# Performance work log

Hardware: AMD Instinct MI355X
Metric: run time of the kernel (lower is better)

Reference implementation:

```python
import jax, jax.numpy as jnp
import numpy as np

N_NODES = 50000
N_EDGES = 800000
N_FEAT = 128
HID = 128
N_LAYER = 3
FC_HID = 256
N_CLASS = 10
N_GRAPHS = 64


def setup_inputs() -> dict:
    key = jax.random.key(0)
    ks = jax.random.split(key, 10)
    x = jax.random.normal(ks[0], (N_NODES, N_FEAT), dtype=jnp.float32)
    edge_index = jax.random.randint(ks[1], (2, N_EDGES), 0, N_NODES, dtype=jnp.int32)
    batch = jnp.sort(jax.random.randint(ks[2], (N_NODES,), 0, N_GRAPHS, dtype=jnp.int32))
    s = 0.05
    # SAGEConv per layer: lin_l acts on mean-aggregated neighbors, lin_r on root.
    Wl = jax.random.normal(ks[3], (N_LAYER, HID, HID), dtype=jnp.float32) * s
    Wr = jax.random.normal(ks[4], (N_LAYER, HID, HID), dtype=jnp.float32) * s
    bl = jnp.zeros((N_LAYER, HID), dtype=jnp.float32)
    fc1_w = jax.random.normal(ks[5], (HID * N_LAYER, FC_HID), dtype=jnp.float32) * s
    fc1_b = jnp.zeros((FC_HID,), dtype=jnp.float32)
    fc2_w = jax.random.normal(ks[6], (FC_HID, N_CLASS), dtype=jnp.float32) * s
    fc2_b = jnp.zeros((N_CLASS,), dtype=jnp.float32)
    return {"x": x, "edge_index": edge_index, "batch": batch,
            "Wl": Wl, "Wr": Wr, "bl": bl,
            "fc1_w": fc1_w, "fc1_b": fc1_b, "fc2_w": fc2_w, "fc2_b": fc2_b}


def reference(x, edge_index, batch, Wl, Wr, bl, fc1_w, fc1_b, fc2_w, fc2_b):
    # normalize edge indices to start at 0 (as in the torch forward)
    ei = edge_index - jnp.min(edge_index)
    src, dst = ei[0], ei[1]
    # in-degree for mean aggregation (clamped to avoid div-by-zero)
    deg = jax.ops.segment_sum(jnp.ones((src.shape[0],), x.dtype), dst,
                              num_segments=N_NODES)
    inv_deg = 1.0 / jnp.maximum(deg, 1.0)[:, None]  # [N,1]
    h = x
    layer_outs = []
    for i in range(N_LAYER):
        # (dropout is identity in eval mode)
        agg = jax.ops.segment_sum(h[src], dst, num_segments=N_NODES) * inv_deg  # [N,H]
        h = jax.nn.relu(agg @ Wl[i] + h @ Wr[i] + bl[i])
        layer_outs.append(h)
    hcat = jnp.concatenate(layer_outs, axis=1)  # [N, H*n_layer]
    # mean pooling per graph
    counts = jax.ops.segment_sum(jnp.ones((N_NODES,), x.dtype), batch,
                                 num_segments=N_GRAPHS)
    pooled = jax.ops.segment_sum(hcat, batch, num_segments=N_GRAPHS)
    pooled = pooled / jnp.maximum(counts, 1.0)[:, None]  # [G, H*n_layer]
    out = jax.nn.relu(pooled @ fc1_w + fc1_b) @ fc2_w + fc2_b  # [G, n_class]
    return out
```

## Files before the change

### kernel.cpp

```cpp
#include <hip/hip_runtime.h>
#include <hip/hip_bf16.h>
#include <limits.h>

#define N_NODES 50000
#define N_EDGES 800000
#define HID 128
#define N_LAYER 3
#define FC_HID 256
#define N_CLASS 10
#define N_GRAPHS 64
#define NBKT 98
#define BIN_NB 256
#define PER_BLK ((N_EDGES + BIN_NB - 1) / BIN_NB)

typedef __attribute__((ext_vector_type(8))) short short8;
typedef __attribute__((ext_vector_type(4))) float f32x4;

__device__ inline unsigned f2bf(float f) {
    unsigned u = __float_as_uint(f);
    return (u + 0x7FFFu + ((u >> 16) & 1u)) >> 16;
}
__device__ inline float bf2f(unsigned b) { return __uint_as_float(b << 16); }

__global__ __launch_bounds__(512) void k_minh(const int* __restrict__ ei,
                                              int* __restrict__ emin,
                                              int* __restrict__ hist) {
    __shared__ int red[512];
    __shared__ int lh[NBKT];
    int t = threadIdx.x;
    if (t < NBKT) lh[t] = 0;
    __syncthreads();
    int e0 = blockIdx.x * PER_BLK, e1 = min(e0 + PER_BLK, N_EDGES);
    int v = INT_MAX;
    for (int j = e0 + t; j < e1; j += 512) {
        int s = ei[j], d = ei[N_EDGES + j];
        v = min(v, min(s, d));
        atomicAdd(&lh[d >> 9], 1);
    }
    red[t] = v;
    __syncthreads();
    for (int off = 256; off > 0; off >>= 1) {
        if (t < off) red[t] = min(red[t], red[t + off]);
        __syncthreads();
    }
    if (t == 0) atomicMin(emin, red[0]);
    if (t < NBKT) hist[blockIdx.x * NBKT + t] = lh[t];
}

__global__ void k_base(const int* __restrict__ hist, int* __restrict__ colex,
                       int* __restrict__ btot) {
    __shared__ int s[BIN_NB];
    int b = blockIdx.x, t = threadIdx.x;
    int v = hist[t * NBKT + b];
    s[t] = v;
    __syncthreads();
    for (int off = 1; off < BIN_NB; off <<= 1) {
        int u = (t >= off) ? s[t - off] : 0;
        __syncthreads();
        s[t] += u;
        __syncthreads();
    }
    colex[t * NBKT + b] = s[t] - v;
    if (t == BIN_NB - 1) btot[b] = s[t];
}

__global__ void k_bscan(const int* __restrict__ btot, int* __restrict__ bboff,
                        int* __restrict__ rp, const int* __restrict__ batch,
                        float* __restrict__ counts) {
    __shared__ int s[128];
    int t = threadIdx.x;
    int v = (t < NBKT) ? btot[t] : 0;
    s[t] = v;
    __syncthreads();
    for (int off = 1; off < 128; off <<= 1) {
        int u = (t >= off) ? s[t - off] : 0;
        __syncthreads();
        s[t] += u;
        __syncthreads();
    }
    if (t < NBKT) bboff[t] = s[t] - v;
    if (t == 127) { bboff[NBKT] = s[127]; rp[N_NODES] = s[127]; }
    if (t < N_GRAPHS) {
        int g = t;
        int lo = 0, hi = N_NODES;
        while (lo < hi) { int mid = (lo + hi) >> 1; if (batch[mid] < g) lo = mid + 1; else hi = mid; }
        int lb = lo;
        lo = lb; hi = N_NODES;
        while (lo < hi) { int mid = (lo + hi) >> 1; if (batch[mid] <= g) lo = mid + 1; else hi = mid; }
        counts[g] = (float)(lo - lb);
    }
}

__global__ __launch_bounds__(512) void k_bin(const int* __restrict__ ei,
                                             const int* __restrict__ emin,
                                             const int* __restrict__ bboff,
                                             const int* __restrict__ colex,
                                             unsigned* __restrict__ ebuf) {
    __shared__ int lcnt[NBKT];
    __shared__ int lbase[NBKT];
    int t = threadIdx.x, blk = blockIdx.x;
    if (t < NBKT) {
        lcnt[t] = 0;
        lbase[t] = bboff[t] + colex[blk * NBKT + t];
    }
    __syncthreads();
    int m = *emin;
    int e0 = blk * PER_BLK, e1 = min(e0 + PER_BLK, N_EDGES);
    for (int j = e0 + t; j < e1; j += 512) {
        int s = ei[j] - m, d = ei[N_EDGES + j];
        int bk = d >> 9;
        int idx = atomicAdd(&lcnt[bk], 1);
        ebuf[lbase[bk] + idx] = ((unsigned)s << 9) | (unsigned)(d & 511);
    }
}

__global__ __launch_bounds__(512) void k_scatter2(const unsigned* __restrict__ ebuf,
                                                  const int* __restrict__ bboff,
                                                  const int* __restrict__ emin,
                                                  int* __restrict__ rp,
                                                  float* __restrict__ invd,
                                                  int* __restrict__ csr) {
    __shared__ int ldeg[512];
    __shared__ int lsc[512];
    __shared__ int lfill[512];
    int b = blockIdx.x, t = threadIdx.x;
    int m = *emin;
    if (b == NBKT) {
        for (int nd = NBKT * 512 - m + t; nd < N_NODES; nd += 512)
            if (nd >= 0) { rp[nd] = N_EDGES; invd[nd] = 1.0f; }
        return;
    }
    ldeg[t] = 0;
    lfill[t] = 0;
    __syncthreads();
    int beg = bboff[b], end = bboff[b + 1];
    for (int e = beg + t; e < end; e += 512)
        atomicAdd(&ldeg[ebuf[e] & 511], 1);
    __syncthreads();
    int v = ldeg[t];
    lsc[t] = v;
    __syncthreads();
    for (int off = 1; off < 512; off <<= 1) {
        int u = (t >= off) ? lsc[t - off] : 0;
        __syncthreads();
        lsc[t] += u;
        __syncthreads();
    }
    int base = beg + lsc[t] - v;
    lsc[t] = base;
    int nd = (b << 9) + t - m;
    if (nd >= 0 && nd < N_NODES) {
        rp[nd] = base;
        invd[nd] = 1.0f / (float)max(v, 1);
    }
    __syncthreads();
    for (int e = beg + t; e < end; e += 512) {
        unsigned p = ebuf[e];
        int loc = p & 511;
        int pos = lsc[loc] + atomicAdd(&lfill[loc], 1);
        csr[pos] = (int)(p >> 9);
    }
}

__global__ void k_cvt(const float* __restrict__ x, unsigned* __restrict__ xb, int n4) {
    int i = blockIdx.x * blockDim.x + threadIdx.x;
    if (i >= n4) return;
    float4 v = *(const float4*)(x + (size_t)i * 4);
    uint2 o;
    o.x = f2bf(v.x) | (f2bf(v.y) << 16);
    o.y = f2bf(v.z) | (f2bf(v.w) << 16);
    *(uint2*)(xb + (size_t)i * 2) = o;
}

__global__ void k_prep(const float* __restrict__ Wl, const float* __restrict__ Wr,
                       unsigned* __restrict__ wlh, unsigned* __restrict__ wll,
                       unsigned* __restrict__ wrh, unsigned* __restrict__ wrl) {
    int b = blockIdx.x;
    int t = threadIdx.x;
    const float* src = (b < 3) ? (Wl + (size_t)b * HID * HID) : (Wr + (size_t)(b - 3) * HID * HID);
    unsigned* dh = (b < 3) ? (wlh + (size_t)b * HID * 64) : (wrh + (size_t)(b - 3) * HID * 64);
    unsigned* dl = (b < 3) ? (wll + (size_t)b * HID * 64) : (wrl + (size_t)(b - 3) * HID * 64);
    for (int i = 0; i < 32; ++i) {
        int u = t * 32 + i;
        int n = u >> 6, kk = u & 63;
        float v0 = src[(size_t)(2 * kk) * HID + n];
        float v1 = src[(size_t)(2 * kk + 1) * HID + n];
        unsigned h0 = f2bf(v0), h1 = f2bf(v1);
        unsigned l0 = f2bf(v0 - bf2f(h0)), l1 = f2bf(v1 - bf2f(h1));
        dh[u] = h0 | (h1 << 16);
        dl[u] = l0 | (l1 << 16);
    }
}

__global__ void k_agg(const unsigned* __restrict__ hb, const int* __restrict__ rp,
                      const int* __restrict__ csr, const float* __restrict__ invd,
                      unsigned* __restrict__ aggb) {
    const int n = blockIdx.x;
    const int lane = threadIdx.x;
    int beg = rp[n], end = rp[n + 1];
    float p0 = 0, p1 = 0, q0 = 0, q1 = 0, r0 = 0, r1 = 0, t0 = 0, t1 = 0;
    int e = beg;
    for (; e + 8 <= end; e += 8) {
        int s0 = csr[e], s1 = csr[e + 1], s2 = csr[e + 2], s3 = csr[e + 3];
        int s4 = csr[e + 4], s5 = csr[e + 5], s6 = csr[e + 6], s7 = csr[e + 7];
        unsigned u0 = hb[(size_t)s0 * 64 + lane];
        unsigned u1 = hb[(size_t)s1 * 64 + lane];
        unsigned u2 = hb[(size_t)s2 * 64 + lane];
        unsigned u3 = hb[(size_t)s3 * 64 + lane];
        unsigned u4 = hb[(size_t)s4 * 64 + lane];
        unsigned u5 = hb[(size_t)s5 * 64 + lane];
        unsigned u6 = hb[(size_t)s6 * 64 + lane];
        unsigned u7 = hb[(size_t)s7 * 64 + lane];
        p0 += __uint_as_float(u0 << 16); p1 += __uint_as_float(u0 & 0xFFFF0000u);
        q0 += __uint_as_float(u1 << 16); q1 += __uint_as_float(u1 & 0xFFFF0000u);
        r0 += __uint_as_float(u2 << 16); r1 += __uint_as_float(u2 & 0xFFFF0000u);
        t0 += __uint_as_float(u3 << 16); t1 += __uint_as_float(u3 & 0xFFFF0000u);
        p0 += __uint_as_float(u4 << 16); p1 += __uint_as_float(u4 & 0xFFFF0000u);
        q0 += __uint_as_float(u5 << 16); q1 += __uint_as_float(u5 & 0xFFFF0000u);
        r0 += __uint_as_float(u6 << 16); r1 += __uint_as_float(u6 & 0xFFFF0000u);
        t0 += __uint_as_float(u7 << 16); t1 += __uint_as_float(u7 & 0xFFFF0000u);
    }
    for (; e < end; ++e) {
        unsigned u = hb[(size_t)csr[e] * 64 + lane];
        p0 += __uint_as_float(u << 16);
        p1 += __uint_as_float(u & 0xFFFF0000u);
    }
    float iv = invd[n];
    unsigned o = f2bf((p0 + q0 + r0 + t0) * iv) | (f2bf((p1 + q1 + r1 + t1) * iv) << 16);
    aggb[(size_t)n * 64 + lane] = o;
}

__global__ __launch_bounds__(256, 4) void k_gemm(
    const unsigned* __restrict__ aggb, const unsigned* __restrict__ hinb,
    const unsigned* __restrict__ wlh, const unsigned* __restrict__ wll,
    const unsigned* __restrict__ wrh, const unsigned* __restrict__ wrl,
    const float* __restrict__ bias, const int* __restrict__ batch,
    unsigned* __restrict__ houtb, float* __restrict__ pooled, int layer) {
    __shared__ float Ts[64 * 132];
    __shared__ int bs[64];
    const int tx = threadIdx.x;
    const int wave = tx >> 6, lane = tx & 63;
    const int row0 = blockIdx.x * 64;
    const int lrow = lane & 15, kgrp = lane >> 4;

    if (tx < 64) {
        int grow = row0 + tx;
        bs[tx] = (grow < N_NODES) ? batch[grow] : -1;
    }

    f32x4 acc[4][2];
#pragma unroll
    for (int m = 0; m < 4; ++m)
#pragma unroll
        for (int n = 0; n < 2; ++n) acc[m][n] = (f32x4){0.f, 0.f, 0.f, 0.f};
    const short8 zf = {0, 0, 0, 0, 0, 0, 0, 0};

    for (int kc = 0; kc < 4; ++kc) {
        const int koff = kc * 16 + kgrp * 4;
        short8 af[4], hf[4];
#pragma unroll
        for (int m = 0; m < 4; ++m) {
            int r = row0 + m * 16 + lrow;
            if (r < N_NODES) {
                af[m] = *(const short8*)(aggb + (size_t)r * 64 + koff);
                hf[m] = *(const short8*)(hinb + (size_t)r * 64 + koff);
            } else {
                af[m] = zf;
                hf[m] = zf;
            }
        }
#pragma unroll
        for (int n = 0; n < 2; ++n) {
            int wn = wave * 2 + n;
            size_t wbase = (size_t)(wn * 16 + lrow) * 64 + koff;
            short8 fl_h = *(const short8*)(wlh + wbase);
            short8 fl_l = *(const short8*)(wll + wbase);
            short8 fr_h = *(const short8*)(wrh + wbase);
            short8 fr_l = *(const short8*)(wrl + wbase);
#pragma unroll
            for (int m = 0; m < 4; ++m) {
                acc[m][n] = __builtin_amdgcn_mfma_f32_16x16x32_bf16(af[m], fl_h, acc[m][n], 0, 0, 0);
                acc[m][n] = __builtin_amdgcn_mfma_f32_16x16x32_bf16(af[m], fl_l, acc[m][n], 0, 0, 0);
                acc[m][n] = __builtin_amdgcn_mfma_f32_16x16x32_bf16(hf[m], fr_h, acc[m][n], 0, 0, 0);
                acc[m][n] = __builtin_amdgcn_mfma_f32_16x16x32_bf16(hf[m], fr_l, acc[m][n], 0, 0, 0);
            }
        }
    }

#pragma unroll
    for (int n = 0; n < 2; ++n) {
        int c = wave * 32 + n * 16 + lrow;
        float bb = bias[c];
#pragma unroll
        for (int m = 0; m < 4; ++m)
#pragma unroll
            for (int reg = 0; reg < 4; ++reg) {
                int r = m * 16 + kgrp * 4 + reg;
                Ts[r * 132 + c] = fmaxf(acc[m][n][reg] + bb, 0.f);
            }
    }
    __syncthreads();

#pragma unroll
    for (int it = 0; it < 4; ++it) {
        int f = it * 256 + tx;
        int r = f >> 4, slot = f & 15;
        int grow = row0 + r;
        if (grow < N_NODES) {
            const float* ts = &Ts[r * 132 + slot * 8];
            uint4 o;
            o.x = f2bf(ts[0]) | (f2bf(ts[1]) << 16);
            o.y = f2bf(ts[2]) | (f2bf(ts[3]) << 16);
            o.z = f2bf(ts[4]) | (f2bf(ts[5]) << 16);
            o.w = f2bf(ts[6]) | (f2bf(ts[7]) << 16);
            *(uint4*)(houtb + (size_t)grow * 64 + slot * 4) = o;
        }
    }

    if (tx < 128) {
        int j = tx;
        float run = 0.f;
        int curb = bs[0];
        for (int r = 0; r < 64; ++r) {
            int bb = bs[r];
            if (bb != curb) {
                if (curb >= 0)
                    atomicAdd(&pooled[(size_t)curb * (HID * N_LAYER) + layer * HID + j], run);
                run = 0.f;
                curb = bb;
            }
            run += Ts[r * 132 + j];
        }
        if (curb >= 0)
            atomicAdd(&pooled[(size_t)curb * (HID * N_LAYER) + layer * HID + j], run);
    }
}

__global__ void k_fc(const float* __restrict__ pooled, const float* __restrict__ counts,
                     const float* __restrict__ fc1w, const float* __restrict__ fc1b,
                     const float* __restrict__ fc2w, const float* __restrict__ fc2b,
                     float* __restrict__ out) {
    __shared__ float pr[HID * N_LAYER];
    __shared__ float a1[FC_HID];
    const int g = blockIdx.x, t = threadIdx.x;
    float invc = 1.0f / fmaxf(counts[g], 1.0f);
    for (int i = t; i < HID * N_LAYER; i += FC_HID)
        pr[i] = pooled[(size_t)g * (HID * N_LAYER) + i] * invc;
    __syncthreads();
    float acc = fc1b[t];
    for (int k = 0; k < HID * N_LAYER; ++k)
        acc = fmaf(pr[k], fc1w[(size_t)k * FC_HID + t], acc);
    a1[t] = fmaxf(acc, 0.f);
    __syncthreads();
    if (t < N_CLASS) {
        float o = fc2b[t];
        for (int k = 0; k < FC_HID; ++k)
            o = fmaf(a1[k], fc2w[(size_t)k * N_CLASS + t], o);
        out[(size_t)g * N_CLASS + t] = o;
    }
}

extern "C" void kernel_launch(void* const* d_in, const int* in_sizes, int n_in,
                              void* d_out, int out_size, void* d_ws, size_t ws_size,
                              hipStream_t stream) {
    const float* x = (const float*)d_in[0];
    const int* ei = (const int*)d_in[1];
    const int* batch = (const int*)d_in[2];
    const float* Wl = (const float*)d_in[3];
    const float* Wr = (const float*)d_in[4];
    const float* bl = (const float*)d_in[5];
    const float* fc1w = (const float*)d_in[6];
    const float* fc1b = (const float*)d_in[7];
    const float* fc2w = (const float*)d_in[8];
    const float* fc2b = (const float*)d_in[9];
    float* out = (float*)d_out;

    char* ws = (char*)d_ws;
    size_t off = 0;
    auto alloc = [&](size_t bytes) {
        void* p = ws + off;
        off += (bytes + 255) & ~size_t(255);
        return p;
    };
    int* emin = (int*)alloc(4);
    float* pooled = (float*)alloc((size_t)N_GRAPHS * HID * N_LAYER * 4);
    int* hist = (int*)alloc((size_t)BIN_NB * NBKT * 4);
    int* colex = (int*)alloc((size_t)BIN_NB * NBKT * 4);
    int* btot = (int*)alloc(NBKT * 4);
    int* bboff = (int*)alloc((NBKT + 1) * 4);
    int* rp = (int*)alloc((N_NODES + 1) * 4);
    float* invd = (float*)alloc(N_NODES * 4);
    float* counts = (float*)alloc(N_GRAPHS * 4);
    unsigned* ebuf = (unsigned*)alloc((size_t)N_EDGES * 4);
    int* csr = (int*)alloc((size_t)N_EDGES * 4);
    unsigned* wlh = (unsigned*)alloc((size_t)N_LAYER * HID * 64 * 4);
    unsigned* wll = (unsigned*)alloc((size_t)N_LAYER * HID * 64 * 4);
    unsigned* wrh = (unsigned*)alloc((size_t)N_LAYER * HID * 64 * 4);
    unsigned* wrl = (unsigned*)alloc((size_t)N_LAYER * HID * 64 * 4);
    unsigned* aggb = (unsigned*)alloc((size_t)N_NODES * 64 * 4);
    unsigned* xb = (unsigned*)alloc((size_t)N_NODES * 64 * 4);
    unsigned* hb1 = (unsigned*)alloc((size_t)N_NODES * 64 * 4);
    unsigned* hb2 = (unsigned*)alloc((size_t)N_NODES * 64 * 4);

    hipMemsetAsync(emin, 0x7F, 4, stream);
    hipMemsetAsync(pooled, 0, (size_t)N_GRAPHS * HID * N_LAYER * 4, stream);

    k_minh<<<BIN_NB, 512, 0, stream>>>(ei, emin, hist);
    k_base<<<NBKT, BIN_NB, 0, stream>>>(hist, colex, btot);
    k_bscan<<<1, 128, 0, stream>>>(btot, bboff, rp, batch, counts);
    k_bin<<<BIN_NB, 512, 0, stream>>>(ei, emin, bboff, colex, ebuf);
    k_scatter2<<<NBKT + 1, 512, 0, stream>>>(ebuf, bboff, emin, rp, invd, csr);
    k_cvt<<<(N_NODES * HID / 4 + 255) / 256, 256, 0, stream>>>(x, xb, N_NODES * HID / 4);
    k_prep<<<6, 256, 0, stream>>>(Wl, Wr, wlh, wll, wrh, wrl);

    const unsigned* hin = xb;
    unsigned* houts[3] = {hb1, hb2, hb1};
    for (int layer = 0; layer < N_LAYER; ++layer) {
        k_agg<<<N_NODES, 64, 0, stream>>>(hin, rp, csr, invd, aggb);
        k_gemm<<<(N_NODES + 63) / 64, 256, 0, stream>>>(
            aggb, hin,
            wlh + (size_t)layer * HID * 64, wll + (size_t)layer * HID * 64,
            wrh + (size_t)layer * HID * 64, wrl + (size_t)layer * HID * 64,
            bl + (size_t)layer * HID, batch, houts[layer], pooled, layer);
        hin = houts[layer];
    }
    k_fc<<<N_GRAPHS, 256, 0, stream>>>(pooled, counts, fc1w, fc1b, fc2w, fc2b, out);
}
```

Before: 277.2 us.

## Split aggregation by feature quarters with four edge lanes per node

The neighbor-mean aggregation now launches one wave per node per quarter of the feature columns. Each wave's 64 lanes cover 16 columns times 4 interleaved edges, and the partial sums are combined with cross-lane shuffles. This gives each wave more independent edge gathers and finer-grained work to hide gather latency and improve load balance. The cost is 64-byte rather than 256-byte row segments per gather, four times as many reads of the row pointers and CSR indices, and extra shuffle work.

```diff
diff --git a/kernel.cpp b/kernel.cpp
--- a/kernel.cpp
+++ b/kernel.cpp
@@ -12,6 +12,7 @@
 #define NBKT 98
 #define BIN_NB 256
 #define PER_BLK ((N_EDGES + BIN_NB - 1) / BIN_NB)
+#define AGG_NB ((N_NODES + 3) / 4)
 
 typedef __attribute__((ext_vector_type(8))) short short8;
 typedef __attribute__((ext_vector_type(4))) float f32x4;
@@ -192,42 +193,39 @@
     }
 }
 
-__global__ void k_agg(const unsigned* __restrict__ hb, const int* __restrict__ rp,
-                      const int* __restrict__ csr, const float* __restrict__ invd,
-                      unsigned* __restrict__ aggb) {
-    const int n = blockIdx.x;
-    const int lane = threadIdx.x;
+__global__ __launch_bounds__(256) void k_agg(const unsigned* __restrict__ hb,
+                                             const int* __restrict__ rp,
+                                             const int* __restrict__ csr,
+                                             const float* __restrict__ invd,
+                                             unsigned* __restrict__ aggb) {
+    const int tx = threadIdx.x;
+    const int wave = tx >> 6, lane = tx & 63;
+    const int q = blockIdx.x / AGG_NB;
+    const int nb = blockIdx.x % AGG_NB;
+    const int n = nb * 4 + wave;
+    const int sub = lane >> 4, fl = lane & 15;
+    const int col = q * 16 + fl;
     int beg = rp[n], end = rp[n + 1];
-    float p0 = 0, p1 = 0, q0 = 0, q1 = 0, r0 = 0, r1 = 0, t0 = 0, t1 = 0;
-    int e = beg;
-    for (; e + 8 <= end; e += 8) {
-        int s0 = csr[e], s1 = csr[e + 1], s2 = csr[e + 2], s3 = csr[e + 3];
-        int s4 = csr[e + 4], s5 = csr[e + 5], s6 = csr[e + 6], s7 = csr[e + 7];
-        unsigned u0 = hb[(size_t)s0 * 64 + lane];
-        unsigned u1 = hb[(size_t)s1 * 64 + lane];
-        unsigned u2 = hb[(size_t)s2 * 64 + lane];
-        unsigned u3 = hb[(size_t)s3 * 64 + lane];
-        unsigned u4 = hb[(size_t)s4 * 64 + lane];
-        unsigned u5 = hb[(size_t)s5 * 64 + lane];
-        unsigned u6 = hb[(size_t)s6 * 64 + lane];
-        unsigned u7 = hb[(size_t)s7 * 64 + lane];
-        p0 += __uint_as_float(u0 << 16); p1 += __uint_as_float(u0 & 0xFFFF0000u);
-        q0 += __uint_as_float(u1 << 16); q1 += __uint_as_float(u1 & 0xFFFF0000u);
-        r0 += __uint_as_float(u2 << 16); r1 += __uint_as_float(u2 & 0xFFFF0000u);
-        t0 += __uint_as_float(u3 << 16); t1 += __uint_as_float(u3 & 0xFFFF0000u);
-        p0 += __uint_as_float(u4 << 16); p1 += __uint_as_float(u4 & 0xFFFF0000u);
-        q0 += __uint_as_float(u5 << 16); q1 += __uint_as_float(u5 & 0xFFFF0000u);
-        r0 += __uint_as_float(u6 << 16); r1 += __uint_as_float(u6 & 0xFFFF0000u);
-        t0 += __uint_as_float(u7 << 16); t1 += __uint_as_float(u7 & 0xFFFF0000u);
-    }
-    for (; e < end; ++e) {
-        unsigned u = hb[(size_t)csr[e] * 64 + lane];
-        p0 += __uint_as_float(u << 16);
-        p1 += __uint_as_float(u & 0xFFFF0000u);
-    }
-    float iv = invd[n];
-    unsigned o = f2bf((p0 + q0 + r0 + t0) * iv) | (f2bf((p1 + q1 + r1 + t1) * iv) << 16);
-    aggb[(size_t)n * 64 + lane] = o;
+    float a0 = 0.f, a1 = 0.f, b0 = 0.f, b1 = 0.f;
+    int e = beg + sub;
+    for (; e + 4 < end; e += 8) {
+        int s0 = csr[e], s1 = csr[e + 4];
+        unsigned u0 = hb[(size_t)s0 * 64 + col];
+        unsigned u1 = hb[(size_t)s1 * 64 + col];
+        a0 += __uint_as_float(u0 << 16); a1 += __uint_as_float(u0 & 0xFFFF0000u);
+        b0 += __uint_as_float(u1 << 16); b1 += __uint_as_float(u1 & 0xFFFF0000u);
+    }
+    for (; e < end; e += 4) {
+        unsigned u = hb[(size_t)csr[e] * 64 + col];
+        a0 += __uint_as_float(u << 16); a1 += __uint_as_float(u & 0xFFFF0000u);
+    }
+    a0 += b0; a1 += b1;
+    a0 += __shfl_xor(a0, 16, 64); a0 += __shfl_xor(a0, 32, 64);
+    a1 += __shfl_xor(a1, 16, 64); a1 += __shfl_xor(a1, 32, 64);
+    if (sub == 0) {
+        float iv = invd[n];
+        aggb[(size_t)n * 64 + col] = f2bf(a0 * iv) | (f2bf(a1 * iv) << 16);
+    }
 }
 
 __global__ __launch_bounds__(256, 4) void k_gemm(
@@ -416,7 +414,7 @@
     const unsigned* hin = xb;
     unsigned* houts[3] = {hb1, hb2, hb1};
     for (int layer = 0; layer < N_LAYER; ++layer) {
-        k_agg<<<N_NODES, 64, 0, stream>>>(hin, rp, csr, invd, aggb);
+        k_agg<<<4 * AGG_NB, 256, 0, stream>>>(hin, rp, csr, invd, aggb);
         k_gemm<<<(N_NODES + 63) / 64, 256, 0, stream>>>(
             aggb, hin,
             wlh + (size_t)layer * HID * 64, wll + (size_t)layer * HID * 64,
```

Result: slower. 433.5 us (+56.4%).

## Fuse neighbor aggregation into GEMM kernel and merge small setup launches

Applied to the files above, without the earlier changes.

Neighbor mean aggregation now runs inside the GEMM kernel: each wave gathers 16 rows into shared memory, and the MFMA loop reads the aggregated tile from LDS instead of a global aggb buffer. This removes three k_agg launches and the global round trip of the aggregated features. Setup is also consolidated: the per-block edge minimum is written out and reduced in k_bscan instead of atomically, pooled is zeroed in k_base, and the two memsets are dropped. The x conversion and weight prep are merged into one launch. The trade-off is that the fused kernel has only 782 blocks doing the latency-bound gather, compared with 50000 small blocks before, so less parallelism is available to hide gather latency.

```diff
diff --git a/kernel.cpp b/kernel.cpp
--- a/kernel.cpp
+++ b/kernel.cpp
@@ -12,6 +12,8 @@
 #define NBKT 98
 #define BIN_NB 256
 #define PER_BLK ((N_EDGES + BIN_NB - 1) / BIN_NB)
+#define GEMM_NB ((N_NODES + 63) / 64)
+#define CVT_NB ((N_NODES * HID / 4 + 255) / 256)
 
 typedef __attribute__((ext_vector_type(8))) short short8;
 typedef __attribute__((ext_vector_type(4))) float f32x4;
@@ -23,7 +25,7 @@
 __device__ inline float bf2f(unsigned b) { return __uint_as_float(b << 16); }
 
 __global__ __launch_bounds__(512) void k_minh(const int* __restrict__ ei,
-                                              int* __restrict__ emin,
+                                              int* __restrict__ bmin,
                                               int* __restrict__ hist) {
     __shared__ int red[512];
     __shared__ int lh[NBKT];
@@ -43,14 +45,16 @@
         if (t < off) red[t] = min(red[t], red[t + off]);
         __syncthreads();
     }
-    if (t == 0) atomicMin(emin, red[0]);
+    if (t == 0) bmin[blockIdx.x] = red[0];
     if (t < NBKT) hist[blockIdx.x * NBKT + t] = lh[t];
 }
 
 __global__ void k_base(const int* __restrict__ hist, int* __restrict__ colex,
-                       int* __restrict__ btot) {
+                       int* __restrict__ btot, float* __restrict__ pooled) {
     __shared__ int s[BIN_NB];
     int b = blockIdx.x, t = threadIdx.x;
+    int gid = b * BIN_NB + t;
+    if (gid < N_GRAPHS * HID * N_LAYER) pooled[gid] = 0.f;
     int v = hist[t * NBKT + b];
     s[t] = v;
     __syncthreads();
@@ -64,11 +68,20 @@
     if (t == BIN_NB - 1) btot[b] = s[t];
 }
 
-__global__ void k_bscan(const int* __restrict__ btot, int* __restrict__ bboff,
-                        int* __restrict__ rp, const int* __restrict__ batch,
+__global__ void k_bscan(const int* __restrict__ btot, const int* __restrict__ bmin,
+                        int* __restrict__ bboff, int* __restrict__ rp,
+                        int* __restrict__ emin, const int* __restrict__ batch,
                         float* __restrict__ counts) {
     __shared__ int s[128];
+    __shared__ int s2[128];
     int t = threadIdx.x;
+    s2[t] = min(bmin[t], bmin[t + 128]);
+    __syncthreads();
+    for (int off = 64; off > 0; off >>= 1) {
+        if (t < off) s2[t] = min(s2[t], s2[t + off]);
+        __syncthreads();
+    }
+    if (t == 0) *emin = s2[0];
     int v = (t < NBKT) ? btot[t] : 0;
     s[t] = v;
     __syncthreads();
@@ -162,82 +175,49 @@
     }
 }
 
-__global__ void k_cvt(const float* __restrict__ x, unsigned* __restrict__ xb, int n4) {
-    int i = blockIdx.x * blockDim.x + threadIdx.x;
-    if (i >= n4) return;
-    float4 v = *(const float4*)(x + (size_t)i * 4);
-    uint2 o;
-    o.x = f2bf(v.x) | (f2bf(v.y) << 16);
-    o.y = f2bf(v.z) | (f2bf(v.w) << 16);
-    *(uint2*)(xb + (size_t)i * 2) = o;
-}
-
-__global__ void k_prep(const float* __restrict__ Wl, const float* __restrict__ Wr,
-                       unsigned* __restrict__ wlh, unsigned* __restrict__ wll,
-                       unsigned* __restrict__ wrh, unsigned* __restrict__ wrl) {
-    int b = blockIdx.x;
-    int t = threadIdx.x;
-    const float* src = (b < 3) ? (Wl + (size_t)b * HID * HID) : (Wr + (size_t)(b - 3) * HID * HID);
-    unsigned* dh = (b < 3) ? (wlh + (size_t)b * HID * 64) : (wrh + (size_t)(b - 3) * HID * 64);
-    unsigned* dl = (b < 3) ? (wll + (size_t)b * HID * 64) : (wrl + (size_t)(b - 3) * HID * 64);
-    for (int i = 0; i < 32; ++i) {
-        int u = t * 32 + i;
-        int n = u >> 6, kk = u & 63;
-        float v0 = src[(size_t)(2 * kk) * HID + n];
-        float v1 = src[(size_t)(2 * kk + 1) * HID + n];
-        unsigned h0 = f2bf(v0), h1 = f2bf(v1);
-        unsigned l0 = f2bf(v0 - bf2f(h0)), l1 = f2bf(v1 - bf2f(h1));
-        dh[u] = h0 | (h1 << 16);
-        dl[u] = l0 | (l1 << 16);
-    }
-}
-
-__global__ void k_agg(const unsigned* __restrict__ hb, const int* __restrict__ rp,
-                      const int* __restrict__ csr, const float* __restrict__ invd,
-                      unsigned* __restrict__ aggb) {
-    const int n = blockIdx.x;
-    const int lane = threadIdx.x;
-    int beg = rp[n], end = rp[n + 1];
-    float p0 = 0, p1 = 0, q0 = 0, q1 = 0, r0 = 0, r1 = 0, t0 = 0, t1 = 0;
-    int e = beg;
-    for (; e + 8 <= end; e += 8) {
-        int s0 = csr[e], s1 = csr[e + 1], s2 = csr[e + 2], s3 = csr[e + 3];
-        int s4 = csr[e + 4], s5 = csr[e + 5], s6 = csr[e + 6], s7 = csr[e + 7];
-        unsigned u0 = hb[(size_t)s0 * 64 + lane];
-        unsigned u1 = hb[(size_t)s1 * 64 + lane];
-        unsigned u2 = hb[(size_t)s2 * 64 + lane];
-        unsigned u3 = hb[(size_t)s3 * 64 + lane];
-        unsigned u4 = hb[(size_t)s4 * 64 + lane];
-        unsigned u5 = hb[(size_t)s5 * 64 + lane];
-        unsigned u6 = hb[(size_t)s6 * 64 + lane];
-        unsigned u7 = hb[(size_t)s7 * 64 + lane];
-        p0 += __uint_as_float(u0 << 16); p1 += __uint_as_float(u0 & 0xFFFF0000u);
-        q0 += __uint_as_float(u1 << 16); q1 += __uint_as_float(u1 & 0xFFFF0000u);
-        r0 += __uint_as_float(u2 << 16); r1 += __uint_as_float(u2 & 0xFFFF0000u);
-        t0 += __uint_as_float(u3 << 16); t1 += __uint_as_float(u3 & 0xFFFF0000u);
-        p0 += __uint_as_float(u4 << 16); p1 += __uint_as_float(u4 & 0xFFFF0000u);
-        q0 += __uint_as_float(u5 << 16); q1 += __uint_as_float(u5 & 0xFFFF0000u);
-        r0 += __uint_as_float(u6 << 16); r1 += __uint_as_float(u6 & 0xFFFF0000u);
-        t0 += __uint_as_float(u7 << 16); t1 += __uint_as_float(u7 & 0xFFFF0000u);
-    }
-    for (; e < end; ++e) {
-        unsigned u = hb[(size_t)csr[e] * 64 + lane];
-        p0 += __uint_as_float(u << 16);
-        p1 += __uint_as_float(u & 0xFFFF0000u);
-    }
-    float iv = invd[n];
-    unsigned o = f2bf((p0 + q0 + r0 + t0) * iv) | (f2bf((p1 + q1 + r1 + t1) * iv) << 16);
-    aggb[(size_t)n * 64 + lane] = o;
-}
-
-__global__ __launch_bounds__(256, 4) void k_gemm(
-    const unsigned* __restrict__ aggb, const unsigned* __restrict__ hinb,
+__global__ void k_cvtprep(const float* __restrict__ x, unsigned* __restrict__ xb,
+                          const float* __restrict__ Wl, const float* __restrict__ Wr,
+                          unsigned* __restrict__ wlh, unsigned* __restrict__ wll,
+                          unsigned* __restrict__ wrh, unsigned* __restrict__ wrl) {
+    int b = blockIdx.x, t = threadIdx.x;
+    if (b < 6) {
+        const float* src = (b < 3) ? (Wl + (size_t)b * HID * HID) : (Wr + (size_t)(b - 3) * HID * HID);
+        unsigned* dh = (b < 3) ? (wlh + (size_t)b * HID * 64) : (wrh + (size_t)(b - 3) * HID * 64);
+        unsigned* dl = (b < 3) ? (wll + (size_t)b * HID * 64) : (wrl + (size_t)(b - 3) * HID * 64);
+        for (int i = 0; i < 32; ++i) {
+            int u = t * 32 + i;
+            int n = u >> 6, kk = u & 63;
+            float v0 = src[(size_t)(2 * kk) * HID + n];
+            float v1 = src[(size_t)(2 * kk + 1) * HID + n];
+            unsigned h0 = f2bf(v0), h1 = f2bf(v1);
+            unsigned l0 = f2bf(v0 - bf2f(h0)), l1 = f2bf(v1 - bf2f(h1));
+            dh[u] = h0 | (h1 << 16);
+            dl[u] = l0 | (l1 << 16);
+        }
+    } else {
+        int i = (b - 6) * 256 + t;
+        if (i < N_NODES * HID / 4) {
+            float4 v = *(const float4*)(x + (size_t)i * 4);
+            uint2 o;
+            o.x = f2bf(v.x) | (f2bf(v.y) << 16);
+            o.y = f2bf(v.z) | (f2bf(v.w) << 16);
+            *(uint2*)(xb + (size_t)i * 2) = o;
+        }
+    }
+}
+
+__global__ __launch_bounds__(256, 4) void k_gfused(
+    const unsigned* __restrict__ hinb,
+    const int* __restrict__ rp, const int* __restrict__ csr,
+    const float* __restrict__ invd,
     const unsigned* __restrict__ wlh, const unsigned* __restrict__ wll,
     const unsigned* __restrict__ wrh, const unsigned* __restrict__ wrl,
     const float* __restrict__ bias, const int* __restrict__ batch,
     unsigned* __restrict__ houtb, float* __restrict__ pooled, int layer) {
-    __shared__ float Ts[64 * 132];
+    __shared__ float smem[64 * 132];
     __shared__ int bs[64];
+    unsigned* Al = (unsigned*)smem;
+    float* Ts = smem;
     const int tx = threadIdx.x;
     const int wave = tx >> 6, lane = tx & 63;
     const int row0 = blockIdx.x * 64;
@@ -248,6 +228,46 @@
         bs[tx] = (grow < N_NODES) ? batch[grow] : -1;
     }
 
+    for (int i = 0; i < 16; ++i) {
+        int r = wave * 16 + i;
+        int n = row0 + r;
+        unsigned o = 0u;
+        if (n < N_NODES) {
+            int beg = rp[n], end = rp[n + 1];
+            float p0 = 0, p1 = 0, q0 = 0, q1 = 0, r0 = 0, r1 = 0, t0 = 0, t1 = 0;
+            int e = beg;
+            for (; e + 8 <= end; e += 8) {
+                int s0 = csr[e], s1 = csr[e + 1], s2 = csr[e + 2], s3 = csr[e + 3];
+                int s4 = csr[e + 4], s5 = csr[e + 5], s6 = csr[e + 6], s7 = csr[e + 7];
+                unsigned u0 = hinb[(size_t)s0 * 64 + lane];
+                unsigned u1 = hinb[(size_t)s1 * 64 + lane];
+                unsigned u2 = hinb[(size_t)s2 * 64 + lane];
+                unsigned u3 = hinb[(size_t)s3 * 64 + lane];
+                unsigned u4 = hinb[(size_t)s4 * 64 + lane];
+                unsigned u5 = hinb[(size_t)s5 * 64 + lane];
+                unsigned u6 = hinb[(size_t)s6 * 64 + lane];
+                unsigned u7 = hinb[(size_t)s7 * 64 + lane];
+                p0 += __uint_as_float(u0 << 16); p1 += __uint_as_float(u0 & 0xFFFF0000u);
+                q0 += __uint_as_float(u1 << 16); q1 += __uint_as_float(u1 & 0xFFFF0000u);
+                r0 += __uint_as_float(u2 << 16); r1 += __uint_as_float(u2 & 0xFFFF0000u);
+                t0 += __uint_as_float(u3 << 16); t1 += __uint_as_float(u3 & 0xFFFF0000u);
+                p0 += __uint_as_float(u4 << 16); p1 += __uint_as_float(u4 & 0xFFFF0000u);
+                q0 += __uint_as_float(u5 << 16); q1 += __uint_as_float(u5 & 0xFFFF0000u);
+                r0 += __uint_as_float(u6 << 16); r1 += __uint_as_float(u6 & 0xFFFF0000u);
+                t0 += __uint_as_float(u7 << 16); t1 += __uint_as_float(u7 & 0xFFFF0000u);
+            }
+            for (; e < end; ++e) {
+                unsigned u = hinb[(size_t)csr[e] * 64 + lane];
+                p0 += __uint_as_float(u << 16);
+                p1 += __uint_as_float(u & 0xFFFF0000u);
+            }
+            float iv = invd[n];
+            o = f2bf((p0 + q0 + r0 + t0) * iv) | (f2bf((p1 + q1 + r1 + t1) * iv) << 16);
+        }
+        Al[r * 68 + lane] = o;
+    }
+    __syncthreads();
+
     f32x4 acc[4][2];
 #pragma unroll
     for (int m = 0; m < 4; ++m)
@@ -260,14 +280,10 @@
         short8 af[4], hf[4];
 #pragma unroll
         for (int m = 0; m < 4; ++m) {
-            int r = row0 + m * 16 + lrow;
-            if (r < N_NODES) {
-                af[m] = *(const short8*)(aggb + (size_t)r * 64 + koff);
-                hf[m] = *(const short8*)(hinb + (size_t)r * 64 + koff);
-            } else {
-                af[m] = zf;
-                hf[m] = zf;
-            }
+            int rr = m * 16 + lrow;
+            af[m] = *(const short8*)&Al[rr * 68 + koff];
+            int grow = row0 + rr;
+            hf[m] = (grow < N_NODES) ? *(const short8*)(hinb + (size_t)grow * 64 + koff) : zf;
         }
 #pragma unroll
         for (int n = 0; n < 2; ++n) {
@@ -286,6 +302,7 @@
             }
         }
     }
+    __syncthreads();
 
 #pragma unroll
     for (int n = 0; n < 2; ++n) {
@@ -383,6 +400,7 @@
         return p;
     };
     int* emin = (int*)alloc(4);
+    int* bmin = (int*)alloc(BIN_NB * 4);
     float* pooled = (float*)alloc((size_t)N_GRAPHS * HID * N_LAYER * 4);
     int* hist = (int*)alloc((size_t)BIN_NB * NBKT * 4);
     int* colex = (int*)alloc((size_t)BIN_NB * NBKT * 4);
@@ -397,28 +415,22 @@
     unsigned* wll = (unsigned*)alloc((size_t)N_LAYER * HID * 64 * 4);
     unsigned* wrh = (unsigned*)alloc((size_t)N_LAYER * HID * 64 * 4);
     unsigned* wrl = (unsigned*)alloc((size_t)N_LAYER * HID * 64 * 4);
-    unsigned* aggb = (unsigned*)alloc((size_t)N_NODES * 64 * 4);
     unsigned* xb = (unsigned*)alloc((size_t)N_NODES * 64 * 4);
     unsigned* hb1 = (unsigned*)alloc((size_t)N_NODES * 64 * 4);
     unsigned* hb2 = (unsigned*)alloc((size_t)N_NODES * 64 * 4);
 
-    hipMemsetAsync(emin, 0x7F, 4, stream);
-    hipMemsetAsync(pooled, 0, (size_t)N_GRAPHS * HID * N_LAYER * 4, stream);
-
-    k_minh<<<BIN_NB, 512, 0, stream>>>(ei, emin, hist);
-    k_base<<<NBKT, BIN_NB, 0, stream>>>(hist, colex, btot);
-    k_bscan<<<1, 128, 0, stream>>>(btot, bboff, rp, batch, counts);
+    k_minh<<<BIN_NB, 512, 0, stream>>>(ei, bmin, hist);
+    k_base<<<NBKT, BIN_NB, 0, stream>>>(hist, colex, btot, pooled);
+    k_bscan<<<1, 128, 0, stream>>>(btot, bmin, bboff, rp, emin, batch, counts);
     k_bin<<<BIN_NB, 512, 0, stream>>>(ei, emin, bboff, colex, ebuf);
     k_scatter2<<<NBKT + 1, 512, 0, stream>>>(ebuf, bboff, emin, rp, invd, csr);
-    k_cvt<<<(N_NODES * HID / 4 + 255) / 256, 256, 0, stream>>>(x, xb, N_NODES * HID / 4);
-    k_prep<<<6, 256, 0, stream>>>(Wl, Wr, wlh, wll, wrh, wrl);
+    k_cvtprep<<<6 + CVT_NB, 256, 0, stream>>>(x, xb, Wl, Wr, wlh, wll, wrh, wrl);
 
     const unsigned* hin = xb;
     unsigned* houts[3] = {hb1, hb2, hb1};
     for (int layer = 0; layer < N_LAYER; ++layer) {
-        k_agg<<<N_NODES, 64, 0, stream>>>(hin, rp, csr, invd, aggb);
-        k_gemm<<<(N_NODES + 63) / 64, 256, 0, stream>>>(
-            aggb, hin,
+        k_gfused<<<GEMM_NB, 256, 0, stream>>>(
+            hin, rp, csr, invd,
             wlh + (size_t)layer * HID * 64, wll + (size_t)layer * HID * 64,
             wrh + (size_t)layer * HID * 64, wrl + (size_t)layer * HID * 64,
             bl + (size_t)layer * HID, batch, houts[layer], pooled, layer);
```

New measurement: 351.8 us. +26.9%, slower.
